# Performance work log

Measured on AMD Instinct MI355X. Metric: run time of the kernel, lower is better.

Reference implementation:

```python
import jax, jax.numpy as jnp
import numpy as np

N_STEPS = 3000
DT = 0.02


def make_phi_t(n=N_STEPS, dt=DT):
    # Central-difference first-derivative operator with one-sided 2nd-order ends.
    P = np.zeros((n, n), dtype=np.float32)
    P[0, 0:3] = [-1.5, 2.0, -0.5]
    idx = np.arange(1, n - 1)
    P[idx, idx - 1] = -0.5
    P[idx, idx + 1] = 0.5
    P[n - 1, n - 3:] = [0.5, -2.0, 1.5]
    return jnp.asarray(P / dt)


def lstm_layer(x, w_ih, w_hh, b_ih, b_hh):
    # x: [B, T, I]; PyTorch gate order i, f, g, o along the 4H axis.
    B, T, _ = x.shape
    H = w_hh.shape[1]
    x_proj = jnp.einsum('bti,gi->btg', x, w_ih) + b_ih + b_hh  # [B, T, 4H]

    def step(carry, xt):
        h, c = carry
        gates = xt + h @ w_hh.T  # [B, 4H]
        i, f, g, o = jnp.split(gates, 4, axis=-1)
        c = jax.nn.sigmoid(f) * c + jax.nn.sigmoid(i) * jnp.tanh(g)
        h = jax.nn.sigmoid(o) * jnp.tanh(c)
        return (h, c), h

    h0 = jnp.zeros((B, H), x.dtype)
    (_, _), hs = jax.lax.scan(step, (h0, h0), x_proj.transpose(1, 0, 2))
    return hs.transpose(1, 0, 2)  # [B, T, H]


def setup_inputs() -> dict:
    key = jax.random.key(0)
    B, T, I, H = 64, N_STEPS, 8, 128
    ks = jax.random.split(key, 16)
    s = lambda k, shape, fan: (jax.random.normal(k, shape, jnp.float32) / np.sqrt(fan)).astype(jnp.float32)
    return {
        'x': jax.random.normal(ks[0], (B, T, I), jnp.float32),
        'w_ih0': s(ks[1], (4 * H, I), I), 'w_hh0': s(ks[2], (4 * H, H), H),
        'b_ih0': s(ks[3], (4 * H,), H), 'b_hh0': s(ks[4], (4 * H,), H),
        'w_ih1': s(ks[5], (4 * H, H), H), 'w_hh1': s(ks[6], (4 * H, H), H),
        'b_ih1': s(ks[7], (4 * H,), H), 'b_hh1': s(ks[8], (4 * H,), H),
        'fc1_w': s(ks[9], (16, H), H), 'fc1_b': s(ks[10], (16,), H),
        'fc2_w': s(ks[11], (4, 16), 16), 'fc2_b': s(ks[12], (4,), 16),
        'fc3_w': s(ks[13], (1, 4), 4), 'fc3_b': s(ks[14], (1,), 4),
    }


def reference(x, w_ih0, w_hh0, b_ih0, b_hh0, w_ih1, w_hh1, b_ih1, b_hh1,
              fc1_w, fc1_b, fc2_w, fc2_b, fc3_w, fc3_b):
    phi = make_phi_t()  # fixed [3000, 3000] FD operator (buffer, not learned)
    h = lstm_layer(x, w_ih0, w_hh0, b_ih0, b_hh0)
    h = lstm_layer(h, w_ih1, w_hh1, b_ih1, b_hh1)
    h = jax.nn.relu(h @ fc1_w.T + fc1_b)
    h = jax.nn.relu(h @ fc2_w.T + fc2_b)
    y = h @ fc3_w.T + fc3_b            # [B, T, 1]
    yt = y[:, :, 0].T                  # [T, B]
    x_tt = phi @ (phi @ yt)            # double derivative via dense matmuls
    return x_tt.T[:, :, None]          # [B, T, 1]
```

## Files before the change

kernel.cpp:

```cpp
#include <hip/hip_runtime.h>
#include <math.h>


#define T_STEPS 3000
#define BATCH   64
#define HID     128
#define INV_DT  50.0f

__device__ __forceinline__ float sigmoid_(float x) {
    return 1.0f / (1.0f + __expf(-x));
}
__device__ __forceinline__ float tanh_(float x) {
    return 1.0f - 2.0f / (__expf(2.0f * x) + 1.0f);
}

__global__ void __launch_bounds__(512)
lstm_layer0(const float* __restrict__ x,
            const float* __restrict__ w_ih,
            const float* __restrict__ w_hh,
            const float* __restrict__ b_ih,
            const float* __restrict__ b_hh,
            float* __restrict__ h_out)
{
    const int b   = blockIdx.x;
    const int tid = threadIdx.x;
    const int j   = tid >> 2;
    const int q   = tid & 3;
    const int kq  = q * 32;

    __shared__ __align__(16) float4 Wl4[8 * 512];
    __shared__ __align__(16) float  h_pad[2][160];

    float w[96];
#pragma unroll
    for (int g = 0; g < 3; ++g) {
#pragma unroll
        for (int i = 0; i < 32; i += 4) {
            float4 v = *(const float4*)(w_hh + (size_t)(g * HID + j) * HID + kq + i);
            w[g*32 + i] = v.x; w[g*32 + i+1] = v.y; w[g*32 + i+2] = v.z; w[g*32 + i+3] = v.w;
        }
    }
#pragma unroll
    for (int i = 0; i < 8; ++i)
        Wl4[i * 512 + tid] = *(const float4*)(w_hh + (size_t)(3 * HID + j) * HID + kq + 4 * i);

    float wi[8];
#pragma unroll
    for (int i = 0; i < 8; i += 4) {
        float4 v = *(const float4*)(w_ih + (size_t)(q * HID + j) * 8 + i);
        wi[i] = v.x; wi[i+1] = v.y; wi[i+2] = v.z; wi[i+3] = v.w;
    }
    const float bias = b_ih[q * HID + j] + b_hh[q * HID + j];
    float c = 0.0f;

    if (tid < 160) h_pad[0][tid] = 0.0f;
    __syncthreads();

    const float* xrow = x + (size_t)b * T_STEPS * 8;
    float* hb = h_out + (size_t)b * T_STEPS * HID;

#pragma unroll 1
    for (int t = 0; t < T_STEPS; ++t) {
        const int rb = t & 1;
        float4 xa = *(const float4*)(xrow + t * 8);
        float4 xc = *(const float4*)(xrow + t * 8 + 4);
        float xterm = bias
                    + wi[0]*xa.x + wi[1]*xa.y + wi[2]*xa.z + wi[3]*xa.w
                    + wi[4]*xc.x + wi[5]*xc.y + wi[6]*xc.z + wi[7]*xc.w;

        float a0 = 0.f, a1 = 0.f, a2 = 0.f, a3 = 0.f;
        const float* hq = &h_pad[rb][40 * q];
#pragma unroll
        for (int i = 0; i < 8; ++i) {
            float4 hv = *(const float4*)(hq + 4 * i);
            float4 g4 = Wl4[i * 512 + tid];
            a0 += w[     4*i]*hv.x + w[     4*i+1]*hv.y + w[     4*i+2]*hv.z + w[     4*i+3]*hv.w;
            a1 += w[32 + 4*i]*hv.x + w[32 + 4*i+1]*hv.y + w[32 + 4*i+2]*hv.z + w[32 + 4*i+3]*hv.w;
            a2 += w[64 + 4*i]*hv.x + w[64 + 4*i+1]*hv.y + w[64 + 4*i+2]*hv.z + w[64 + 4*i+3]*hv.w;
            a3 += g4.x*hv.x + g4.y*hv.y + g4.z*hv.z + g4.w*hv.w;
        }
        float s0 = __shfl_xor((q & 1) ? a0 : a1, 1);
        float s1 = __shfl_xor((q & 1) ? a2 : a3, 1);
        float p0 = ((q & 1) ? a1 : a0) + s0;
        float p1 = ((q & 1) ? a3 : a2) + s1;
        float S  = ((q & 2) ? p1 : p0) + __shfl_xor((q & 2) ? p0 : p1, 2);
        S += xterm;

        float av = (q == 2) ? tanh_(S) : sigmoid_(S);
        float t1 = __shfl_xor(av, 1);
        float t2 = __shfl_xor(av, 2);
        float t3 = __shfl_xor(t1, 2);
        if (q == 0) {
            c = t1 * c + av * t2;
            float h = t3 * tanh_(c);
            h_pad[rb ^ 1][(j & 31) + 40 * (j >> 5)] = h;
            hb[(size_t)t * HID + j] = h;
        }
        __syncthreads();
    }
}

__global__ void __launch_bounds__(512)
xp_proj(const float* __restrict__ w_ih,
        const float* __restrict__ b_ih,
        const float* __restrict__ b_hh,
        const float* __restrict__ h1,
        float* __restrict__ xp)
{
    const int blk = blockIdx.x;
    const int b   = blk / 125;
    const int t0  = (blk % 125) * 24;
    const int r   = threadIdx.x;

    float acc[24];
    const float bias = b_ih[r] + b_hh[r];
#pragma unroll
    for (int u = 0; u < 24; ++u) acc[u] = bias;

    const float* hp = h1 + ((size_t)b * T_STEPS + t0) * HID;
    const float* wr = w_ih + (size_t)r * HID;
#pragma unroll 2
    for (int k4 = 0; k4 < 32; ++k4) {
        float4 w4 = *(const float4*)(wr + 4 * k4);
#pragma unroll
        for (int u = 0; u < 24; ++u) {
            float4 h4 = *(const float4*)(hp + u * HID + 4 * k4);
            acc[u] += w4.x*h4.x + w4.y*h4.y + w4.z*h4.z + w4.w*h4.w;
        }
    }
    float* xo = xp + ((size_t)b * T_STEPS + t0) * 512 + r;
#pragma unroll
    for (int u = 0; u < 24; ++u) xo[(size_t)u * 512] = acc[u];
}

__global__ void __launch_bounds__(512)
lstm_layer1_pre(const float* __restrict__ w_hh,
                const float* __restrict__ xp,
                float* __restrict__ h_buf)
{
    const int b   = blockIdx.x;
    const int tid = threadIdx.x;
    const int j   = tid >> 2;
    const int q   = tid & 3;
    const int kq  = q * 32;

    __shared__ __align__(16) float4 Wl4[8 * 512];
    __shared__ __align__(16) float  h_pad[2][160];

    float w[96];
#pragma unroll
    for (int g = 0; g < 3; ++g) {
#pragma unroll
        for (int i = 0; i < 32; i += 4) {
            float4 v = *(const float4*)(w_hh + (size_t)(g * HID + j) * HID + kq + i);
            w[g*32 + i] = v.x; w[g*32 + i+1] = v.y; w[g*32 + i+2] = v.z; w[g*32 + i+3] = v.w;
        }
    }
#pragma unroll
    for (int i = 0; i < 8; ++i)
        Wl4[i * 512 + tid] = *(const float4*)(w_hh + (size_t)(3 * HID + j) * HID + kq + 4 * i);

    float c = 0.0f;
    if (tid < 160) h_pad[0][tid] = 0.0f;
    __syncthreads();

    float* hb = h_buf + (size_t)b * T_STEPS * HID;
    const float* xpb = xp + (size_t)b * T_STEPS * 512 + q * HID + j;

    float xq = xpb[0];
#pragma unroll 1
    for (int t = 0; t < T_STEPS; ++t) {
        const int rb = t & 1;
        const int tn = (t + 1 < T_STEPS) ? t + 1 : t;
        float xq_n = xpb[(size_t)tn * 512];

        float a0 = 0.f, a1 = 0.f, a2 = 0.f, a3 = 0.f;
        const float* hq = &h_pad[rb][40 * q];
#pragma unroll
        for (int i = 0; i < 8; ++i) {
            float4 hv = *(const float4*)(hq + 4 * i);
            float4 g4 = Wl4[i * 512 + tid];
            a0 += w[     4*i]*hv.x + w[     4*i+1]*hv.y + w[     4*i+2]*hv.z + w[     4*i+3]*hv.w;
            a1 += w[32 + 4*i]*hv.x + w[32 + 4*i+1]*hv.y + w[32 + 4*i+2]*hv.z + w[32 + 4*i+3]*hv.w;
            a2 += w[64 + 4*i]*hv.x + w[64 + 4*i+1]*hv.y + w[64 + 4*i+2]*hv.z + w[64 + 4*i+3]*hv.w;
            a3 += g4.x*hv.x + g4.y*hv.y + g4.z*hv.z + g4.w*hv.w;
        }
        float s0 = __shfl_xor((q & 1) ? a0 : a1, 1);
        float s1 = __shfl_xor((q & 1) ? a2 : a3, 1);
        float p0 = ((q & 1) ? a1 : a0) + s0;
        float p1 = ((q & 1) ? a3 : a2) + s1;
        float S  = ((q & 2) ? p1 : p0) + __shfl_xor((q & 2) ? p0 : p1, 2);
        S += xq;

        float av = (q == 2) ? tanh_(S) : sigmoid_(S);
        float t1 = __shfl_xor(av, 1);
        float t2 = __shfl_xor(av, 2);
        float t3 = __shfl_xor(t1, 2);
        if (q == 0) {
            c = t1 * c + av * t2;
            float h = t3 * tanh_(c);
            h_pad[rb ^ 1][(j & 31) + 40 * (j >> 5)] = h;
            hb[(size_t)t * HID + j] = h;
        }
        xq = xq_n;
        __syncthreads();
    }
}

#define CHUNK   10
__global__ void __launch_bounds__(512)
lstm_layer1_fused(const float* __restrict__ w_ih,
                  const float* __restrict__ w_hh,
                  const float* __restrict__ b_ih,
                  const float* __restrict__ b_hh,
                  float* __restrict__ h_buf)
{
    const int b   = blockIdx.x;
    const int tid = threadIdx.x;
    const int j   = tid >> 2;
    const int gt  = tid & 3;
    const int r   = gt * HID + j;
    const int rot = (tid & 7) << 2;

    __shared__ __align__(16) float Wl[512 * 64];
    __shared__ __align__(16) float h_s[2][HID];

    float w[64];
#pragma unroll
    for (int i = 0; i < 64; i += 4) {
        float4 v = *(const float4*)(w_hh + (size_t)r * HID + i);
        w[i] = v.x; w[i+1] = v.y; w[i+2] = v.z; w[i+3] = v.w;
    }
#pragma unroll
    for (int i = 0; i < 64; i += 4) {
        float4 v = *(const float4*)(w_hh + (size_t)r * HID + 64 + i);
        *(float4*)&Wl[tid * 64 + (i ^ rot)] = v;
    }
    const float bias = b_ih[r] + b_hh[r];
    float c = 0.0f;
    if (tid < HID) h_s[0][tid] = 0.0f;
    __syncthreads();

    float* hbB = h_buf + (size_t)b * T_STEPS * HID;
    const float* wihr = w_ih + (size_t)r * HID;

    for (int t0 = 0; t0 < T_STEPS; t0 += CHUNK) {
        float acc[CHUNK];
#pragma unroll
        for (int tau = 0; tau < CHUNK; ++tau) acc[tau] = bias;
        const float* hp = hbB + (size_t)t0 * HID;
#pragma unroll 2
        for (int k4 = 0; k4 < 32; ++k4) {
            float4 w4 = *(const float4*)(wihr + 4 * k4);
#pragma unroll
            for (int tau = 0; tau < CHUNK; ++tau) {
                float4 h4 = *(const float4*)(hp + tau * HID + 4 * k4);
                acc[tau] += w4.x*h4.x + w4.y*h4.y + w4.z*h4.z + w4.w*h4.w;
            }
        }
        __syncthreads();

#pragma unroll
        for (int tt = 0; tt < CHUNK; ++tt) {
            const int rb = tt & 1;
            float a0 = acc[tt];
            float a1 = 0.f, a2 = 0.f, a3 = 0.f;
            float b0 = 0.f, b1 = 0.f, b2 = 0.f, b3 = 0.f;
#pragma unroll
            for (int k4 = 0; k4 < 16; k4 += 4) {
                float4 h0 = *(const float4*)(&h_s[rb][4*k4]);
                float4 h1 = *(const float4*)(&h_s[rb][4*k4 + 4]);
                float4 h2 = *(const float4*)(&h_s[rb][4*k4 + 8]);
                float4 h3 = *(const float4*)(&h_s[rb][4*k4 + 12]);
                a0 += w[4*k4   ]*h0.x + w[4*k4+ 1]*h0.y + w[4*k4+ 2]*h0.z + w[4*k4+ 3]*h0.w;
                a1 += w[4*k4+ 4]*h1.x + w[4*k4+ 5]*h1.y + w[4*k4+ 6]*h1.z + w[4*k4+ 7]*h1.w;
                a2 += w[4*k4+ 8]*h2.x + w[4*k4+ 9]*h2.y + w[4*k4+10]*h2.z + w[4*k4+11]*h2.w;
                a3 += w[4*k4+12]*h3.x + w[4*k4+13]*h3.y + w[4*k4+14]*h3.z + w[4*k4+15]*h3.w;
            }
            {
                const float* wlp = &Wl[tid * 64];
#pragma unroll
                for (int i = 0; i < 64; i += 16) {
                    float4 g0 = *(const float4*)(wlp + ((i     ) ^ rot));
                    float4 g1 = *(const float4*)(wlp + ((i +  4) ^ rot));
                    float4 g2 = *(const float4*)(wlp + ((i +  8) ^ rot));
                    float4 g3 = *(const float4*)(wlp + ((i + 12) ^ rot));
                    float4 h0 = *(const float4*)(&h_s[rb][64 + i]);
                    float4 h1 = *(const float4*)(&h_s[rb][64 + i + 4]);
                    float4 h2 = *(const float4*)(&h_s[rb][64 + i + 8]);
                    float4 h3 = *(const float4*)(&h_s[rb][64 + i + 12]);
                    b0 += g0.x*h0.x + g0.y*h0.y + g0.z*h0.z + g0.w*h0.w;
                    b1 += g1.x*h1.x + g1.y*h1.y + g1.z*h1.z + g1.w*h1.w;
                    b2 += g2.x*h2.x + g2.y*h2.y + g2.z*h2.z + g2.w*h2.w;
                    b3 += g3.x*h3.x + g3.y*h3.y + g3.z*h3.z + g3.w*h3.w;
                }
            }
            float acs = ((a0 + a1) + (a2 + a3)) + ((b0 + b1) + (b2 + b3));

            float av = (gt == 2) ? tanh_(acs) : sigmoid_(acs);
            float t1 = __shfl_xor(av, 1);
            float t2 = __shfl_xor(av, 2);
            float t3 = __shfl_xor(t1, 2);
            if (gt == 0) {
                c = t1 * c + av * t2;
                float h = t3 * tanh_(c);
                h_s[rb ^ 1][j] = h;
                hbB[(size_t)(t0 + tt) * HID + j] = h;
            }
            __syncthreads();
        }
    }
}

__global__ void __launch_bounds__(256)
fc_head(const float* __restrict__ h_buf,
        const float* __restrict__ fc1_w, const float* __restrict__ fc1_b,
        const float* __restrict__ fc2_w, const float* __restrict__ fc2_b,
        const float* __restrict__ fc3_w, const float* __restrict__ fc3_b,
        float* __restrict__ y_bt)
{
    __shared__ __align__(16) float w1[16 * HID];
    __shared__ float sb[89];
    const int tid = threadIdx.x;
    for (int i = tid; i < 16 * HID; i += 256) w1[i] = fc1_w[i];
    if (tid < 16) sb[tid]      = fc1_b[tid];
    if (tid < 64) sb[16 + tid] = fc2_w[tid];
    if (tid < 4)  sb[80 + tid] = fc2_b[tid];
    if (tid < 4)  sb[84 + tid] = fc3_w[tid];
    if (tid == 0) sb[88]       = fc3_b[0];
    __syncthreads();

    const int idx = blockIdx.x * 256 + tid;
    if (idx >= BATCH * T_STEPS) return;
    const float* h = h_buf + (size_t)idx * HID;

    float y1[16];
#pragma unroll
    for (int jo = 0; jo < 16; ++jo) y1[jo] = sb[jo];
#pragma unroll 4
    for (int k4 = 0; k4 < 32; ++k4) {
        float4 hv = *(const float4*)(h + 4 * k4);
#pragma unroll
        for (int jo = 0; jo < 16; ++jo) {
            float4 wv = *(const float4*)(&w1[jo * HID + 4 * k4]);
            y1[jo] += wv.x*hv.x + wv.y*hv.y + wv.z*hv.z + wv.w*hv.w;
        }
    }
    float y2[4];
#pragma unroll
    for (int jo = 0; jo < 4; ++jo) {
        float a = sb[80 + jo];
#pragma unroll
        for (int k = 0; k < 16; ++k) a += sb[16 + jo * 16 + k] * fmaxf(y1[k], 0.0f);
        y2[jo] = fmaxf(a, 0.0f);
    }
    float y = sb[88];
#pragma unroll
    for (int k = 0; k < 4; ++k) y += sb[84 + k] * y2[k];

    y_bt[idx] = y;
}

__global__ void deriv_k(const float* __restrict__ in,
                        float* __restrict__ outp)
{
    const int idx = blockIdx.x * blockDim.x + threadIdx.x;
    if (idx >= BATCH * T_STEPS) return;
    const int t = idx % T_STEPS;
    float v;
    if (t == 0) {
        v = (-1.5f * in[idx] + 2.0f * in[idx + 1] - 0.5f * in[idx + 2]) * INV_DT;
    } else if (t == T_STEPS - 1) {
        v = (0.5f * in[idx - 2] - 2.0f * in[idx - 1] + 1.5f * in[idx]) * INV_DT;
    } else {
        v = (in[idx + 1] - in[idx - 1]) * (0.5f * INV_DT);
    }
    outp[idx] = v;
}

extern "C" void kernel_launch(void* const* d_in, const int* in_sizes, int n_in,
                              void* d_out, int out_size, void* d_ws, size_t ws_size,
                              hipStream_t stream)
{
    const float* x     = (const float*)d_in[0];
    const float* w_ih0 = (const float*)d_in[1];
    const float* w_hh0 = (const float*)d_in[2];
    const float* b_ih0 = (const float*)d_in[3];
    const float* b_hh0 = (const float*)d_in[4];
    const float* w_ih1 = (const float*)d_in[5];
    const float* w_hh1 = (const float*)d_in[6];
    const float* b_ih1 = (const float*)d_in[7];
    const float* b_hh1 = (const float*)d_in[8];
    const float* fc1_w = (const float*)d_in[9];
    const float* fc1_b = (const float*)d_in[10];
    const float* fc2_w = (const float*)d_in[11];
    const float* fc2_b = (const float*)d_in[12];
    const float* fc3_w = (const float*)d_in[13];
    const float* fc3_b = (const float*)d_in[14];
    float* out = (float*)d_out;

    float* h_buf = (float*)d_ws;
    float* y_bt  = (float*)((char*)d_ws + 98304000);
    float* z_bt  = (float*)((char*)d_ws + 98304000 + 768000);
    float* xp    = (float*)((char*)d_ws + 98304000 + 1536000);
    const bool use_pre = ws_size >= (size_t)98304000 + 1536000 + 393216000;

    lstm_layer0<<<dim3(BATCH), dim3(512), 0, stream>>>(x, w_ih0, w_hh0, b_ih0, b_hh0, h_buf);

    if (use_pre) {
        xp_proj<<<dim3(BATCH * 125), dim3(512), 0, stream>>>(w_ih1, b_ih1, b_hh1, h_buf, xp);
        lstm_layer1_pre<<<dim3(BATCH), dim3(512), 0, stream>>>(w_hh1, xp, h_buf);
    } else {
        lstm_layer1_fused<<<dim3(BATCH), dim3(512), 0, stream>>>(w_ih1, w_hh1, b_ih1, b_hh1, h_buf);
    }

    const int nelem = T_STEPS * BATCH;
    fc_head<<<dim3(nelem / 256), dim3(256), 0, stream>>>(
        h_buf, fc1_w, fc1_b, fc2_w, fc2_b, fc3_w, fc3_b, y_bt);
    deriv_k<<<dim3(nelem / 256), dim3(256), 0, stream>>>(y_bt, z_bt);
    deriv_k<<<dim3(nelem / 256), dim3(256), 0, stream>>>(z_bt, out);
}
```

Before: 14.08 ms.

## Fuse layer-1 input projection into recurrent kernel and move gate weights to LDS

Drops the separate xp_proj kernel and its large precomputed projection buffer. Layer 1 now computes the input projection in chunks of 8 timesteps inside the recurrent kernel, using the same quad-split gate layout as layer 0. In both LSTM kernels, the g-gate recurrent weights move from registers to LDS alongside the o-gate weights, which cuts register pressure but adds shared-memory reads on every step. The goal is to avoid the large global memory round trip for xp; the cost is extra serial work inside the latency-bound recurrent loop.

```diff
diff --git a/kernel.cpp b/kernel.cpp
--- a/kernel.cpp
+++ b/kernel.cpp
@@ -5,6 +5,7 @@
 #define T_STEPS 3000
 #define BATCH   64
 #define HID     128
+#define CHUNK   8
 #define INV_DT  50.0f
 
 __device__ __forceinline__ float sigmoid_(float x) {
@@ -28,12 +29,13 @@
     const int q   = tid & 3;
     const int kq  = q * 32;
 
-    __shared__ __align__(16) float4 Wl4[8 * 512];
+    __shared__ __align__(16) float4 WlG[8 * 512];
+    __shared__ __align__(16) float4 WlO[8 * 512];
     __shared__ __align__(16) float  h_pad[2][160];
 
-    float w[96];
-#pragma unroll
-    for (int g = 0; g < 3; ++g) {
+    float w[64];
+#pragma unroll
+    for (int g = 0; g < 2; ++g) {
 #pragma unroll
         for (int i = 0; i < 32; i += 4) {
             float4 v = *(const float4*)(w_hh + (size_t)(g * HID + j) * HID + kq + i);
@@ -41,9 +43,10 @@
         }
     }
 #pragma unroll
-    for (int i = 0; i < 8; ++i)
-        Wl4[i * 512 + tid] = *(const float4*)(w_hh + (size_t)(3 * HID + j) * HID + kq + 4 * i);
-
+    for (int i = 0; i < 8; ++i) {
+        WlG[i * 512 + tid] = *(const float4*)(w_hh + (size_t)(2 * HID + j) * HID + kq + 4 * i);
+        WlO[i * 512 + tid] = *(const float4*)(w_hh + (size_t)(3 * HID + j) * HID + kq + 4 * i);
+    }
     float wi[8];
 #pragma unroll
     for (int i = 0; i < 8; i += 4) {
@@ -73,11 +76,12 @@
 #pragma unroll
         for (int i = 0; i < 8; ++i) {
             float4 hv = *(const float4*)(hq + 4 * i);
-            float4 g4 = Wl4[i * 512 + tid];
+            float4 g2 = WlG[i * 512 + tid];
+            float4 g3 = WlO[i * 512 + tid];
             a0 += w[     4*i]*hv.x + w[     4*i+1]*hv.y + w[     4*i+2]*hv.z + w[     4*i+3]*hv.w;
             a1 += w[32 + 4*i]*hv.x + w[32 + 4*i+1]*hv.y + w[32 + 4*i+2]*hv.z + w[32 + 4*i+3]*hv.w;
-            a2 += w[64 + 4*i]*hv.x + w[64 + 4*i+1]*hv.y + w[64 + 4*i+2]*hv.z + w[64 + 4*i+3]*hv.w;
-            a3 += g4.x*hv.x + g4.y*hv.y + g4.z*hv.z + g4.w*hv.w;
+            a2 += g2.x*hv.x + g2.y*hv.y + g2.z*hv.z + g2.w*hv.w;
+            a3 += g3.x*hv.x + g3.y*hv.y + g3.z*hv.z + g3.w*hv.w;
         }
         float s0 = __shfl_xor((q & 1) ? a0 : a1, 1);
         float s1 = __shfl_xor((q & 1) ? a2 : a3, 1);
@@ -101,42 +105,11 @@
 }
 
 __global__ void __launch_bounds__(512)
-xp_proj(const float* __restrict__ w_ih,
-        const float* __restrict__ b_ih,
-        const float* __restrict__ b_hh,
-        const float* __restrict__ h1,
-        float* __restrict__ xp)
-{
-    const int blk = blockIdx.x;
-    const int b   = blk / 125;
-    const int t0  = (blk % 125) * 24;
-    const int r   = threadIdx.x;
-
-    float acc[24];
-    const float bias = b_ih[r] + b_hh[r];
-#pragma unroll
-    for (int u = 0; u < 24; ++u) acc[u] = bias;
-
-    const float* hp = h1 + ((size_t)b * T_STEPS + t0) * HID;
-    const float* wr = w_ih + (size_t)r * HID;
-#pragma unroll 2
-    for (int k4 = 0; k4 < 32; ++k4) {
-        float4 w4 = *(const float4*)(wr + 4 * k4);
-#pragma unroll
-        for (int u = 0; u < 24; ++u) {
-            float4 h4 = *(const float4*)(hp + u * HID + 4 * k4);
-            acc[u] += w4.x*h4.x + w4.y*h4.y + w4.z*h4.z + w4.w*h4.w;
-        }
-    }
-    float* xo = xp + ((size_t)b * T_STEPS + t0) * 512 + r;
-#pragma unroll
-    for (int u = 0; u < 24; ++u) xo[(size_t)u * 512] = acc[u];
-}
-
-__global__ void __launch_bounds__(512)
-lstm_layer1_pre(const float* __restrict__ w_hh,
-                const float* __restrict__ xp,
-                float* __restrict__ h_buf)
+lstm_layer1(const float* __restrict__ w_ih,
+            const float* __restrict__ w_hh,
+            const float* __restrict__ b_ih,
+            const float* __restrict__ b_hh,
+            float* __restrict__ h_buf)
 {
     const int b   = blockIdx.x;
     const int tid = threadIdx.x;
@@ -144,12 +117,13 @@
     const int q   = tid & 3;
     const int kq  = q * 32;
 
-    __shared__ __align__(16) float4 Wl4[8 * 512];
+    __shared__ __align__(16) float4 WlG[8 * 512];
+    __shared__ __align__(16) float4 WlO[8 * 512];
     __shared__ __align__(16) float  h_pad[2][160];
 
-    float w[96];
-#pragma unroll
-    for (int g = 0; g < 3; ++g) {
+    float w[64];
+#pragma unroll
+    for (int g = 0; g < 2; ++g) {
 #pragma unroll
         for (int i = 0; i < 32; i += 4) {
             float4 v = *(const float4*)(w_hh + (size_t)(g * HID + j) * HID + kq + i);
@@ -157,93 +131,19 @@
         }
     }
 #pragma unroll
-    for (int i = 0; i < 8; ++i)
-        Wl4[i * 512 + tid] = *(const float4*)(w_hh + (size_t)(3 * HID + j) * HID + kq + 4 * i);
-
+    for (int i = 0; i < 8; ++i) {
+        WlG[i * 512 + tid] = *(const float4*)(w_hh + (size_t)(2 * HID + j) * HID + kq + 4 * i);
+        WlO[i * 512 + tid] = *(const float4*)(w_hh + (size_t)(3 * HID + j) * HID + kq + 4 * i);
+    }
+    const float bias = b_ih[q * HID + j] + b_hh[q * HID + j];
     float c = 0.0f;
     if (tid < 160) h_pad[0][tid] = 0.0f;
     __syncthreads();
 
-    float* hb = h_buf + (size_t)b * T_STEPS * HID;
-    const float* xpb = xp + (size_t)b * T_STEPS * 512 + q * HID + j;
-
-    float xq = xpb[0];
+    float* hbB = h_buf + (size_t)b * T_STEPS * HID;
+    const float* wihr = w_ih + (size_t)(q * HID + j) * HID;
+
 #pragma unroll 1
-    for (int t = 0; t < T_STEPS; ++t) {
-        const int rb = t & 1;
-        const int tn = (t + 1 < T_STEPS) ? t + 1 : t;
-        float xq_n = xpb[(size_t)tn * 512];
-
-        float a0 = 0.f, a1 = 0.f, a2 = 0.f, a3 = 0.f;
-        const float* hq = &h_pad[rb][40 * q];
-#pragma unroll
-        for (int i = 0; i < 8; ++i) {
-            float4 hv = *(const float4*)(hq + 4 * i);
-            float4 g4 = Wl4[i * 512 + tid];
-            a0 += w[     4*i]*hv.x + w[     4*i+1]*hv.y + w[     4*i+2]*hv.z + w[     4*i+3]*hv.w;
-            a1 += w[32 + 4*i]*hv.x + w[32 + 4*i+1]*hv.y + w[32 + 4*i+2]*hv.z + w[32 + 4*i+3]*hv.w;
-            a2 += w[64 + 4*i]*hv.x + w[64 + 4*i+1]*hv.y + w[64 + 4*i+2]*hv.z + w[64 + 4*i+3]*hv.w;
-            a3 += g4.x*hv.x + g4.y*hv.y + g4.z*hv.z + g4.w*hv.w;
-        }
-        float s0 = __shfl_xor((q & 1) ? a0 : a1, 1);
-        float s1 = __shfl_xor((q & 1) ? a2 : a3, 1);
-        float p0 = ((q & 1) ? a1 : a0) + s0;
-        float p1 = ((q & 1) ? a3 : a2) + s1;
-        float S  = ((q & 2) ? p1 : p0) + __shfl_xor((q & 2) ? p0 : p1, 2);
-        S += xq;
-
-        float av = (q == 2) ? tanh_(S) : sigmoid_(S);
-        float t1 = __shfl_xor(av, 1);
-        float t2 = __shfl_xor(av, 2);
-        float t3 = __shfl_xor(t1, 2);
-        if (q == 0) {
-            c = t1 * c + av * t2;
-            float h = t3 * tanh_(c);
-            h_pad[rb ^ 1][(j & 31) + 40 * (j >> 5)] = h;
-            hb[(size_t)t * HID + j] = h;
-        }
-        xq = xq_n;
-        __syncthreads();
-    }
-}
-
-#define CHUNK   10
-__global__ void __launch_bounds__(512)
-lstm_layer1_fused(const float* __restrict__ w_ih,
-                  const float* __restrict__ w_hh,
-                  const float* __restrict__ b_ih,
-                  const float* __restrict__ b_hh,
-                  float* __restrict__ h_buf)
-{
-    const int b   = blockIdx.x;
-    const int tid = threadIdx.x;
-    const int j   = tid >> 2;
-    const int gt  = tid & 3;
-    const int r   = gt * HID + j;
-    const int rot = (tid & 7) << 2;
-
-    __shared__ __align__(16) float Wl[512 * 64];
-    __shared__ __align__(16) float h_s[2][HID];
-
-    float w[64];
-#pragma unroll
-    for (int i = 0; i < 64; i += 4) {
-        float4 v = *(const float4*)(w_hh + (size_t)r * HID + i);
-        w[i] = v.x; w[i+1] = v.y; w[i+2] = v.z; w[i+3] = v.w;
-    }
-#pragma unroll
-    for (int i = 0; i < 64; i += 4) {
-        float4 v = *(const float4*)(w_hh + (size_t)r * HID + 64 + i);
-        *(float4*)&Wl[tid * 64 + (i ^ rot)] = v;
-    }
-    const float bias = b_ih[r] + b_hh[r];
-    float c = 0.0f;
-    if (tid < HID) h_s[0][tid] = 0.0f;
-    __syncthreads();
-
-    float* hbB = h_buf + (size_t)b * T_STEPS * HID;
-    const float* wihr = w_ih + (size_t)r * HID;
-
     for (int t0 = 0; t0 < T_STEPS; t0 += CHUNK) {
         float acc[CHUNK];
 #pragma unroll
@@ -263,48 +163,33 @@
 #pragma unroll
         for (int tt = 0; tt < CHUNK; ++tt) {
             const int rb = tt & 1;
-            float a0 = acc[tt];
-            float a1 = 0.f, a2 = 0.f, a3 = 0.f;
-            float b0 = 0.f, b1 = 0.f, b2 = 0.f, b3 = 0.f;
-#pragma unroll
-            for (int k4 = 0; k4 < 16; k4 += 4) {
-                float4 h0 = *(const float4*)(&h_s[rb][4*k4]);
-                float4 h1 = *(const float4*)(&h_s[rb][4*k4 + 4]);
-                float4 h2 = *(const float4*)(&h_s[rb][4*k4 + 8]);
-                float4 h3 = *(const float4*)(&h_s[rb][4*k4 + 12]);
-                a0 += w[4*k4   ]*h0.x + w[4*k4+ 1]*h0.y + w[4*k4+ 2]*h0.z + w[4*k4+ 3]*h0.w;
-                a1 += w[4*k4+ 4]*h1.x + w[4*k4+ 5]*h1.y + w[4*k4+ 6]*h1.z + w[4*k4+ 7]*h1.w;
-                a2 += w[4*k4+ 8]*h2.x + w[4*k4+ 9]*h2.y + w[4*k4+10]*h2.z + w[4*k4+11]*h2.w;
-                a3 += w[4*k4+12]*h3.x + w[4*k4+13]*h3.y + w[4*k4+14]*h3.z + w[4*k4+15]*h3.w;
+            float a0 = 0.f, a1 = 0.f, a2 = 0.f, a3 = 0.f;
+            const float* hq = &h_pad[rb][40 * q];
+#pragma unroll
+            for (int i = 0; i < 8; ++i) {
+                float4 hv = *(const float4*)(hq + 4 * i);
+                float4 g2 = WlG[i * 512 + tid];
+                float4 g3 = WlO[i * 512 + tid];
+                a0 += w[     4*i]*hv.x + w[     4*i+1]*hv.y + w[     4*i+2]*hv.z + w[     4*i+3]*hv.w;
+                a1 += w[32 + 4*i]*hv.x + w[32 + 4*i+1]*hv.y + w[32 + 4*i+2]*hv.z + w[32 + 4*i+3]*hv.w;
+                a2 += g2.x*hv.x + g2.y*hv.y + g2.z*hv.z + g2.w*hv.w;
+                a3 += g3.x*hv.x + g3.y*hv.y + g3.z*hv.z + g3.w*hv.w;
             }
-            {
-                const float* wlp = &Wl[tid * 64];
-#pragma unroll
-                for (int i = 0; i < 64; i += 16) {
-                    float4 g0 = *(const float4*)(wlp + ((i     ) ^ rot));
-                    float4 g1 = *(const float4*)(wlp + ((i +  4) ^ rot));
-                    float4 g2 = *(const float4*)(wlp + ((i +  8) ^ rot));
-                    float4 g3 = *(const float4*)(wlp + ((i + 12) ^ rot));
-                    float4 h0 = *(const float4*)(&h_s[rb][64 + i]);
-                    float4 h1 = *(const float4*)(&h_s[rb][64 + i + 4]);
-                    float4 h2 = *(const float4*)(&h_s[rb][64 + i + 8]);
-                    float4 h3 = *(const float4*)(&h_s[rb][64 + i + 12]);
-                    b0 += g0.x*h0.x + g0.y*h0.y + g0.z*h0.z + g0.w*h0.w;
-                    b1 += g1.x*h1.x + g1.y*h1.y + g1.z*h1.z + g1.w*h1.w;
-                    b2 += g2.x*h2.x + g2.y*h2.y + g2.z*h2.z + g2.w*h2.w;
-                    b3 += g3.x*h3.x + g3.y*h3.y + g3.z*h3.z + g3.w*h3.w;
-                }
-            }
-            float acs = ((a0 + a1) + (a2 + a3)) + ((b0 + b1) + (b2 + b3));
-
-            float av = (gt == 2) ? tanh_(acs) : sigmoid_(acs);
+            float s0 = __shfl_xor((q & 1) ? a0 : a1, 1);
+            float s1 = __shfl_xor((q & 1) ? a2 : a3, 1);
+            float p0 = ((q & 1) ? a1 : a0) + s0;
+            float p1 = ((q & 1) ? a3 : a2) + s1;
+            float S  = ((q & 2) ? p1 : p0) + __shfl_xor((q & 2) ? p0 : p1, 2);
+            S += acc[tt];
+
+            float av = (q == 2) ? tanh_(S) : sigmoid_(S);
             float t1 = __shfl_xor(av, 1);
             float t2 = __shfl_xor(av, 2);
             float t3 = __shfl_xor(t1, 2);
-            if (gt == 0) {
+            if (q == 0) {
                 c = t1 * c + av * t2;
                 float h = t3 * tanh_(c);
-                h_s[rb ^ 1][j] = h;
+                h_pad[rb ^ 1][(j & 31) + 40 * (j >> 5)] = h;
                 hbB[(size_t)(t0 + tt) * HID + j] = h;
             }
             __syncthreads();
@@ -402,17 +287,9 @@
     float* h_buf = (float*)d_ws;
     float* y_bt  = (float*)((char*)d_ws + 98304000);
     float* z_bt  = (float*)((char*)d_ws + 98304000 + 768000);
-    float* xp    = (float*)((char*)d_ws + 98304000 + 1536000);
-    const bool use_pre = ws_size >= (size_t)98304000 + 1536000 + 393216000;
 
     lstm_layer0<<<dim3(BATCH), dim3(512), 0, stream>>>(x, w_ih0, w_hh0, b_ih0, b_hh0, h_buf);
-
-    if (use_pre) {
-        xp_proj<<<dim3(BATCH * 125), dim3(512), 0, stream>>>(w_ih1, b_ih1, b_hh1, h_buf, xp);
-        lstm_layer1_pre<<<dim3(BATCH), dim3(512), 0, stream>>>(w_hh1, xp, h_buf);
-    } else {
-        lstm_layer1_fused<<<dim3(BATCH), dim3(512), 0, stream>>>(w_ih1, w_hh1, b_ih1, b_hh1, h_buf);
-    }
+    lstm_layer1<<<dim3(BATCH), dim3(512), 0, stream>>>(w_ih1, w_hh1, b_ih1, b_hh1, h_buf);
 
     const int nelem = T_STEPS * BATCH;
     fc_head<<<dim3(nelem / 256), dim3(256), 0, stream>>>(
```

Measured after the change: 13.68 ms. -2.9%, faster.
